# Kernel tuning notes

Measured on AMD Instinct MI355X. Metric: run time of the kernel, lower is better.

The kernel has to match this reference:

```python
import jax, jax.numpy as jnp
import numpy as np

N_HEAD = 16
N_KV_HEADS = 4
N_REP = 4
HEAD_DIM = 128
N_EMBD = 2048
EPS = 1e-5
ROPE_BASE = 10000.0


def setup_inputs() -> dict:
    key = jax.random.key(0)
    ks = jax.random.split(key, 5)
    B, T, C = 2, 2048, N_EMBD
    s = 0.02
    return {
        "x": jax.random.normal(ks[0], (B, T, C), dtype=jnp.float32),
        "wq": jax.random.normal(ks[1], (C, N_HEAD * HEAD_DIM), dtype=jnp.float32) * s,
        "wk": jax.random.normal(ks[2], (C, N_KV_HEADS * HEAD_DIM), dtype=jnp.float32) * s,
        "wv": jax.random.normal(ks[3], (C, N_KV_HEADS * HEAD_DIM), dtype=jnp.float32) * s,
        "wc": jax.random.normal(ks[4], (C, C), dtype=jnp.float32) * s,
        "q_norm_w": jnp.ones((HEAD_DIM,), dtype=jnp.float32),
        "k_norm_w": jnp.ones((HEAD_DIM,), dtype=jnp.float32),
    }


def _rmsnorm(x, w):
    # norm in fp32, scale by weight (matches RMSNorm.forward)
    xf = x.astype(jnp.float32)
    rms = jax.lax.rsqrt(jnp.mean(xf * xf, axis=-1, keepdims=True) + EPS)
    return (xf * rms).astype(x.dtype) * w


def _rope(x, cos, sin):
    # x: [B,T,H,D]; cos/sin: [T, D//2]; interleaved even/odd rotation
    xf = x.astype(jnp.float32)
    xe = xf[..., 0::2]
    xo = xf[..., 1::2]
    c = cos[None, :, None, :]
    s = sin[None, :, None, :]
    ye = xe * c - xo * s
    yo = xe * s + xo * c
    y = jnp.stack((ye, yo), axis=-1).reshape(x.shape)
    return y.astype(x.dtype)


def reference(x, wq, wk, wv, wc, q_norm_w, k_norm_w):
    B, T, C = x.shape
    q = (x @ wq).reshape(B, T, N_HEAD, HEAD_DIM)
    k = (x @ wk).reshape(B, T, N_KV_HEADS, HEAD_DIM)
    v = (x @ wv).reshape(B, T, N_KV_HEADS, HEAD_DIM)

    q = _rmsnorm(q, q_norm_w)
    k = _rmsnorm(k, k_norm_w)

    inv_freq = 1.0 / (ROPE_BASE ** (jnp.arange(0, HEAD_DIM, 2, dtype=jnp.float32) / HEAD_DIM))
    theta = jnp.arange(T, dtype=jnp.float32)[:, None] * inv_freq[None, :]  # [T, D//2]
    cos, sin = jnp.cos(theta), jnp.sin(theta)
    q = _rope(q, cos, sin)
    k = _rope(k, cos, sin)

    # GQA: repeat kv heads (repeat_kv with n_rep)
    k = jnp.repeat(k, N_REP, axis=2)  # [B,T,H,D]
    v = jnp.repeat(v, N_REP, axis=2)

    scale = 1.0 / jnp.sqrt(jnp.float32(HEAD_DIM))
    scores = jnp.einsum("bthd,bshd->bhts", q, k) * scale  # [B,H,T,S]
    causal = jnp.tril(jnp.ones((T, T), dtype=bool))
    scores = jnp.where(causal[None, None], scores, jnp.finfo(scores.dtype).min)
    attn = jax.nn.softmax(scores, axis=-1)
    y = jnp.einsum("bhts,bshd->bthd", attn, v).reshape(B, T, C)
    return y @ wc
```

## Files before the change

kernel.cpp:

```cpp
#include <hip/hip_runtime.h>
#include <hip/hip_bf16.h>
#include <cstdint>
#include <cstddef>

using bf16 = __hip_bfloat16;
typedef __attribute__((ext_vector_type(8))) short short8;
typedef __attribute__((ext_vector_type(4))) float f32x4;
typedef __attribute__((ext_vector_type(16))) float f32x16;

#define T_SEQ 2048
#define NHEAD 16
#define NKV 4
#define HD 128
#define CE 2048

__device__ __forceinline__ void gl_lds16(const void* g, void* l) {
  __builtin_amdgcn_global_load_lds(
      (const __attribute__((address_space(1))) unsigned int*)g,
      (__attribute__((address_space(3))) unsigned int*)l, 16, 0, 0);
}

__device__ __forceinline__ unsigned int cvtpk_bf16(float lo, float hi) {
  unsigned int r;
  asm("v_cvt_pk_bf16_f32 %0, %1, %2" : "=v"(r) : "v"(lo), "v"(hi));
  return r;
}

__device__ __forceinline__ void plswap(unsigned int& x, unsigned int& y, int hi) {
#if __has_builtin(__builtin_amdgcn_permlane32_swap)
  auto r = __builtin_amdgcn_permlane32_swap(x, y, false, false);
  x = r[0];
  y = r[1];
#else
  unsigned int xp = (unsigned int)__shfl_xor((int)x, 32);
  unsigned int yp = (unsigned int)__shfl_xor((int)y, 32);
  unsigned int nx = hi ? yp : x;
  unsigned int ny = hi ? y : xp;
  x = nx;
  y = ny;
#endif
}

__global__ void __launch_bounds__(256) cvt_bf16(const float* __restrict__ in,
                                                bf16* __restrict__ out, int n4) {
  const int i = blockIdx.x * blockDim.x + threadIdx.x;
  if (i >= n4) return;
  const float4 v = ((const float4*)in)[i];
  bf16 b0 = __float2bfloat16(v.x), b1 = __float2bfloat16(v.y),
       b2 = __float2bfloat16(v.z), b3 = __float2bfloat16(v.w);
  ushort4 u;
  u.x = *(const unsigned short*)&b0; u.y = *(const unsigned short*)&b1;
  u.z = *(const unsigned short*)&b2; u.w = *(const unsigned short*)&b3;
  ((ushort4*)out)[i] = u;
}

__global__ void __launch_bounds__(256) transpose_cvt(const float* __restrict__ W,
                                                     bf16* __restrict__ Wt, int N) {
  __shared__ float tile[32][33];
  const int tx = threadIdx.x & 31, ty = threadIdx.x >> 5;
  const int bx = blockIdx.x, by = blockIdx.y;
#pragma unroll
  for (int i = 0; i < 4; i++) {
    const int r = by * 32 + ty + i * 8;
    tile[ty + i * 8][tx] = W[(size_t)r * N + bx * 32 + tx];
  }
  __syncthreads();
#pragma unroll
  for (int i = 0; i < 4; i++) {
    const int n = bx * 32 + ty + i * 8;
    Wt[(size_t)n * 2048 + by * 32 + tx] = __float2bfloat16(tile[tx][ty + i * 8]);
  }
}

template <int BM, int BN, int WM, int WN, bool OBF>
__global__ void __launch_bounds__(512, 2)
gemm8i(const bf16* __restrict__ A, const bf16* __restrict__ Bt,
       void* __restrict__ Cv, int M, int N, int K) {
  constexpr int AWS = BM / 2 / WM;
  constexpr int BWS = BN / 2 / WN;
  constexpr int MH = AWS / 16;
  constexpr int NH = BWS / 16;
  constexpr int AH = BM / 128;
  constexpr int BH = BN / 128;
  constexpr int G = 2 * AH + BH;
  __shared__ bf16 smA[2][BM * 64];
  __shared__ bf16 smB[2][BN * 64];

  const int tid = threadIdx.x, lane = tid & 63, wid = tid >> 6;
  const int l15 = lane & 15, l4 = lane >> 4;
  const int wr = wid / WN, wc = wid % WN;

  const int nwg = gridDim.x;
  const int q = nwg >> 3, r = nwg & 7;
  const int xcd = blockIdx.x & 7, lin = blockIdx.x >> 3;
  const int wg = (xcd < r ? xcd * (q + 1) : r * (q + 1) + (xcd - r) * q) + lin;
  const int gw = N / BN;
  const int by = wg / gw, bx = wg % gw;
  const int row0 = by * BM, col0 = bx * BN;
  const int NT = K >> 6;
  const int NI = NT >> 1;

  const bf16* Ag = A + (size_t)row0 * K;
  const bf16* Bg = Bt + (size_t)col0 * K;

  auto stA = [&](int t, int h, int pb) {
    const int k0 = t << 6;
#pragma unroll
    for (int j = 0; j < AH; j++) {
      const int c = (h * AH + j) * 512 + tid;
      const int rowi = c >> 3;
      gl_lds16(Ag + (size_t)rowi * K + k0 + (((c & 7) ^ (rowi & 7)) << 3),
               (void*)(&smA[pb][(size_t)c << 3]));
    }
  };
  auto stB = [&](int t, int h, int pb) {
    const int k0 = t << 6;
#pragma unroll
    for (int j = 0; j < BH; j++) {
      const int c = (h * BH + j) * 512 + tid;
      const int rowi = c >> 3;
      gl_lds16(Bg + (size_t)rowi * K + k0 + (((c & 7) ^ (rowi & 7)) << 3),
               (void*)(&smB[pb][(size_t)c << 3]));
    }
  };
  auto rdA = [&](const bf16* sA, int mh, short8 (&dst)[MH][2]) {
#pragma unroll
    for (int i = 0; i < MH; i++) {
      const int rowl = mh * (BM / 2) + wr * AWS + i * 16 + l15;
#pragma unroll
      for (int kk = 0; kk < 2; kk++)
        dst[i][kk] = *(const short8*)(sA + rowl * 64 +
                                      ((((kk << 2) | l4) ^ (rowl & 7)) << 3));
    }
  };
  auto rdB = [&](const bf16* sB, int nh, short8 (&dst)[NH][2]) {
#pragma unroll
    for (int j = 0; j < NH; j++) {
      const int rowl = nh * (BN / 2) + wc * BWS + j * 16 + l15;
#pragma unroll
      for (int kk = 0; kk < 2; kk++)
        dst[j][kk] = *(const short8*)(sB + rowl * 64 +
                                      ((((kk << 2) | l4) ^ (rowl & 7)) << 3));
    }
  };

  f32x4 acc[2][2][MH][NH];
#pragma unroll
  for (int mh = 0; mh < 2; mh++)
#pragma unroll
    for (int nh = 0; nh < 2; nh++)
#pragma unroll
      for (int i = 0; i < MH; i++)
#pragma unroll
        for (int j = 0; j < NH; j++) acc[mh][nh][i][j] = (f32x4){0.f, 0.f, 0.f, 0.f};

  auto mmq = [&](short8 (&a)[MH][2], short8 (&b)[NH][2], f32x4 (&ac)[MH][NH]) {
    __builtin_amdgcn_s_setprio(1);
#pragma unroll
    for (int i = 0; i < MH; i++)
#pragma unroll
      for (int j = 0; j < NH; j++)
#pragma unroll
        for (int kk = 0; kk < 2; kk++)
          ac[i][j] = __builtin_amdgcn_mfma_f32_16x16x32_bf16(a[i][kk], b[j][kk],
                                                             ac[i][j], 0, 0, 0);
    __builtin_amdgcn_s_setprio(0);
  };

  short8 a0[MH][2], a1[MH][2], b0[NH][2], b1[NH][2];

#define LGKM0_SB                                            \
  asm volatile("s_waitcnt lgkmcnt(0)" ::: "memory");        \
  __builtin_amdgcn_sched_barrier(0);
#define GATE_G                                              \
  asm volatile("s_waitcnt vmcnt(%0)" ::"i"(G) : "memory");

  stA(0, 0, 0); stB(0, 0, 0); stA(0, 1, 0); stB(0, 1, 0);
  stA(1, 0, 1); stB(1, 0, 1); stA(1, 1, 1);
  GATE_G
  __builtin_amdgcn_s_barrier();

  for (int i = 0; i < NI - 1; ++i) {
    const int u = 2 * i, v = u + 1;
    stB(v, 1, 1);
    rdA(smA[0], 0, a0); rdB(smB[0], 0, b0);
    __builtin_amdgcn_s_barrier();
    LGKM0_SB
    mmq(a0, b0, acc[0][0]);
    __builtin_amdgcn_s_barrier();
    stA(u + 2, 0, 0);
    rdA(smA[0], 1, a1);
    __builtin_amdgcn_s_barrier();
    LGKM0_SB
    mmq(a1, b0, acc[1][0]);
    __builtin_amdgcn_s_barrier();
    stB(u + 2, 0, 0);
    rdB(smB[0], 1, b1);
    __builtin_amdgcn_s_barrier();
    LGKM0_SB
    mmq(a1, b1, acc[1][1]);
    __builtin_amdgcn_s_barrier();
    stA(u + 2, 1, 0);
    mmq(a0, b1, acc[0][1]);
    GATE_G
    __builtin_amdgcn_s_barrier();
    stB(u + 2, 1, 0);
    rdA(smA[1], 0, a0); rdB(smB[1], 0, b0);
    __builtin_amdgcn_s_barrier();
    LGKM0_SB
    mmq(a0, b0, acc[0][0]);
    __builtin_amdgcn_s_barrier();
    stA(v + 2, 0, 1);
    rdA(smA[1], 1, a1);
    __builtin_amdgcn_s_barrier();
    LGKM0_SB
    mmq(a1, b0, acc[1][0]);
    __builtin_amdgcn_s_barrier();
    stB(v + 2, 0, 1);
    rdB(smB[1], 1, b1);
    __builtin_amdgcn_s_barrier();
    LGKM0_SB
    mmq(a1, b1, acc[1][1]);
    __builtin_amdgcn_s_barrier();
    stA(v + 2, 1, 1);
    mmq(a0, b1, acc[0][1]);
    GATE_G
    __builtin_amdgcn_s_barrier();
  }

  {
    stB(NT - 1, 1, 1);
    rdA(smA[0], 0, a0); rdB(smB[0], 0, b0);
    __builtin_amdgcn_s_barrier();
    LGKM0_SB
    mmq(a0, b0, acc[0][0]);
    __builtin_amdgcn_s_barrier();
    rdA(smA[0], 1, a1);
    __builtin_amdgcn_s_barrier();
    LGKM0_SB
    mmq(a1, b0, acc[1][0]);
    __builtin_amdgcn_s_barrier();
    rdB(smB[0], 1, b1);
    __builtin_amdgcn_s_barrier();
    LGKM0_SB
    mmq(a1, b1, acc[1][1]);
    __builtin_amdgcn_s_barrier();
    mmq(a0, b1, acc[0][1]);
    asm volatile("s_waitcnt vmcnt(0)" ::: "memory");
    __builtin_amdgcn_s_barrier();
    rdA(smA[1], 0, a0); rdB(smB[1], 0, b0);
    __builtin_amdgcn_s_barrier();
    LGKM0_SB
    mmq(a0, b0, acc[0][0]);
    __builtin_amdgcn_s_barrier();
    rdA(smA[1], 1, a1);
    __builtin_amdgcn_s_barrier();
    LGKM0_SB
    mmq(a1, b0, acc[1][0]);
    __builtin_amdgcn_s_barrier();
    rdB(smB[1], 1, b1);
    __builtin_amdgcn_s_barrier();
    LGKM0_SB
    mmq(a1, b1, acc[1][1]);
    mmq(a0, b1, acc[0][1]);
  }

#pragma unroll
  for (int mh = 0; mh < 2; mh++)
#pragma unroll
    for (int nh = 0; nh < 2; nh++)
#pragma unroll
      for (int i = 0; i < MH; i++)
#pragma unroll
        for (int j = 0; j < NH; j++)
#pragma unroll
          for (int rr = 0; rr < 4; rr++) {
            const size_t row = row0 + mh * (BM / 2) + wr * AWS + i * 16 + l4 * 4 + rr;
            const size_t col = col0 + nh * (BN / 2) + wc * BWS + j * 16 + l15;
            if constexpr (OBF)
              ((bf16*)Cv)[row * N + col] = __float2bfloat16(acc[mh][nh][i][j][rr]);
            else
              ((float*)Cv)[row * N + col] = acc[mh][nh][i][j][rr];
          }
#undef LGKM0_SB
#undef GATE_G
}

__global__ void __launch_bounds__(256) qkv_post(const bf16* __restrict__ QKV,
                                                const float* __restrict__ qw,
                                                const float* __restrict__ kw,
                                                bf16* __restrict__ Qo,
                                                bf16* __restrict__ Ko,
                                                bf16* __restrict__ Vto) {
  const int g = blockIdx.x * 4 + (threadIdx.x >> 6);
  const int lane = threadIdx.x & 63;
  const int hh = g % 24;
  const int bt = g / 24;
  const int b = bt >> 11, t = bt & (T_SEQ - 1);
  int off;
  if (hh < 16) off = hh * 128;
  else if (hh < 20) off = 2048 + (hh - 16) * 128;
  else off = 2560 + (hh - 20) * 128;
  const ushort2 xr = *(const ushort2*)(QKV + (size_t)bt * 3072 + off + lane * 2);
  const float xx = __bfloat162float(*(const bf16*)&xr.x);
  const float xy = __bfloat162float(*(const bf16*)&xr.y);
  if (hh < 20) {
    float ss = xx * xx + xy * xy;
    ss += __shfl_xor(ss, 1);  ss += __shfl_xor(ss, 2);  ss += __shfl_xor(ss, 4);
    ss += __shfl_xor(ss, 8);  ss += __shfl_xor(ss, 16); ss += __shfl_xor(ss, 32);
    const float rms = rsqrtf(ss * (1.0f / 128.0f) + 1e-5f);
    const float* w = (hh < 16) ? qw : kw;
    const float x0 = xx * rms * w[lane * 2];
    const float x1 = xy * rms * w[lane * 2 + 1];
    const float inv = exp2f((float)lane * (-13.287712379549449f / 64.0f));
    const float th = (float)t * inv;
    const float sn = sinf(th), cs = cosf(th);
    const float y0 = x0 * cs - x1 * sn;
    const float y1 = x0 * sn + x1 * cs;
    const bf16 o0 = __float2bfloat16(y0), o1 = __float2bfloat16(y1);
    if (hh < 16) {
      bf16* d = Qo + ((size_t)(b * NHEAD + hh) * T_SEQ + t) * HD + lane * 2;
      d[0] = o0; d[1] = o1;
    } else {
      bf16* d = Ko + ((size_t)(b * NKV + (hh - 16)) * T_SEQ + t) * HD + lane * 2;
      d[0] = o0; d[1] = o1;
    }
  } else {
    bf16* d = Vto + ((size_t)(b * NKV + (hh - 20)) * HD + lane * 2) * T_SEQ + t;
    d[0] = __float2bfloat16(xx);
    d[T_SEQ] = __float2bfloat16(xy);
  }
}

__constant__ unsigned short JT[24] = {
    0x0807, 0x180F, 0x288F, 0x287E,
    0x0706, 0x170D, 0x277D, 0x170E, 0x276C,
    0x0605, 0x160B, 0x266B, 0x160C, 0x265A,
    0x0504, 0x1509, 0x2559, 0x150A, 0x2548,
    0x0403, 0x1408,
    0x0302, 0x0201, 0x0100};

#define ATTN_CL 0.12754125f

__global__ void __launch_bounds__(256, 2) attn_fwd(const bf16* __restrict__ Q,
                                                   const bf16* __restrict__ K,
                                                   const bf16* __restrict__ Vt,
                                                   bf16* __restrict__ Y,
                                                   float* __restrict__ PO,
                                                   float* __restrict__ PML) {
  __shared__ bf16 smK[128 * 128];
  __shared__ bf16 smV[128 * 128];

  const int bid = blockIdx.x;
  const int bh = bid & 31;
  const int jobi = bid >> 5;
  const unsigned int e = JT[jobi];
  const int jq = e & 15;
  const int lo = (e >> 4) & 15;
  const int len = (e >> 8) & 15;
  const int part = e >> 12;
  const int hi_t = lo + len;

  const int h = bh & (NHEAD - 1), b = bh >> 4;
  const int bkv = b * NKV + (h >> 2);

  const int tid = threadIdx.x, wid = tid >> 6, lane = tid & 63;
  const int l31 = lane & 31, hi = lane >> 5;
  const int q0w = jq * 128 + wid * 32;
  const int trow = tid >> 4, tslot = tid & 15;

  const bf16* Kb = K + (size_t)bkv * T_SEQ * HD;
  const bf16* Vb = Vt + (size_t)bkv * HD * T_SEQ;

  const bf16* Qrow = Q + ((size_t)bh * T_SEQ + q0w + l31) * HD + hi * 8;
  short8 qf[8];
#pragma unroll
  for (int ds = 0; ds < 8; ds++) qf[ds] = *(const short8*)(Qrow + ds * 16);

  f32x16 o[4];
#pragma unroll
  for (int d = 0; d < 4; d++) o[d] = (f32x16)(0.f);
  float mrun = -INFINITY, lrun = 0.f;

  constexpr float CL = ATTN_CL;

  for (int t = lo; t < hi_t; t++) {
    const int k0 = t * 128;
    __syncthreads();
#pragma unroll
    for (int i = 0; i < 8; i++) {
      const int row = i * 16 + trow;
      const int ss = (tslot ^ (row & 15)) * 8;
      gl_lds16(Kb + (size_t)(k0 + row) * HD + ss, (void*)((char*)smK + i * 4096 + wid * 1024));
      gl_lds16(Vb + (size_t)row * T_SEQ + k0 + ss, (void*)((char*)smV + i * 4096 + wid * 1024));
    }
    __syncthreads();

    const bool diag = (t == jq);
    const int glim = diag ? wid : 3;

    f32x16 sg[4];
#pragma unroll
    for (int g = 0; g < 4; g++) {
      if (g > glim) continue;
      f32x16 acc = (f32x16)(0.f);
#pragma unroll
      for (int ds = 0; ds < 8; ds++) {
        const int row = g * 32 + l31;
        const short8 kf = *(const short8*)(smK + (size_t)row * 128 +
                                           (((ds << 1) | hi) ^ (row & 15)) * 8);
        acc = __builtin_amdgcn_mfma_f32_32x32x16_bf16(kf, qf[ds], acc, 0, 0, 0);
      }
      sg[g] = acc;
    }
    float tmax = -INFINITY;
#pragma unroll
    for (int g = 0; g < 4; g++) {
      if (g > glim) continue;
      if (diag && g == wid) {
#pragma unroll
        for (int r = 0; r < 16; r++) {
          const int kr = (r & 3) + 8 * (r >> 2) + (hi << 2);
          if (kr > l31) sg[g][r] = -INFINITY;
        }
      }
#pragma unroll
      for (int r = 0; r < 16; r++) tmax = fmaxf(tmax, sg[g][r]);
    }
    tmax = fmaxf(tmax, __shfl_xor(tmax, 32));
    const float mnew = fmaxf(mrun, tmax);
    const float f = exp2f((mrun - mnew) * CL);
    mrun = mnew;
    lrun *= f;
#pragma unroll
    for (int d = 0; d < 4; d++)
#pragma unroll
      for (int r = 0; r < 16; r++) o[d][r] *= f;

    float lsum = 0.f;
#pragma unroll
    for (int g = 0; g < 4; g++) {
      if (g > glim) continue;
      float pp[16];
      float s0 = 0.f, s1 = 0.f;
#pragma unroll
      for (int r = 0; r < 16; r++) pp[r] = exp2f((sg[g][r] - mnew) * CL);
#pragma unroll
      for (int r = 0; r < 8; r++) { s0 += pp[2 * r]; s1 += pp[2 * r + 1]; }
      lsum += s0 + s1;

      unsigned int w0 = cvtpk_bf16(pp[0], pp[1]),  w2 = cvtpk_bf16(pp[4], pp[5]);
      unsigned int w1 = cvtpk_bf16(pp[2], pp[3]),  w3 = cvtpk_bf16(pp[6], pp[7]);
      unsigned int w4 = cvtpk_bf16(pp[8], pp[9]),  w6 = cvtpk_bf16(pp[12], pp[13]);
      unsigned int w5 = cvtpk_bf16(pp[10], pp[11]), w7 = cvtpk_bf16(pp[14], pp[15]);
      plswap(w0, w2, hi); plswap(w1, w3, hi);
      plswap(w4, w6, hi); plswap(w5, w7, hi);
      union { unsigned int u[4]; short8 s8; } pa0, pa1;
      pa0.u[0] = w0; pa0.u[1] = w1; pa0.u[2] = w2; pa0.u[3] = w3;
      pa1.u[0] = w4; pa1.u[1] = w5; pa1.u[2] = w6; pa1.u[3] = w7;

#pragma unroll
      for (int d = 0; d < 4; d++) {
        const int row = d * 32 + l31;
        const int ks0 = g * 2, ks1 = g * 2 + 1;
        const short8 vf0 = *(const short8*)(smV + (size_t)row * 128 +
                                            (((ks0 << 1) | hi) ^ (row & 15)) * 8);
        const short8 vf1 = *(const short8*)(smV + (size_t)row * 128 +
                                            (((ks1 << 1) | hi) ^ (row & 15)) * 8);
        o[d] = __builtin_amdgcn_mfma_f32_32x32x16_bf16(vf0, pa0.s8, o[d], 0, 0, 0);
        o[d] = __builtin_amdgcn_mfma_f32_32x32x16_bf16(vf1, pa1.s8, o[d], 0, 0, 0);
      }
    }
    lrun += lsum + __shfl_xor(lsum, 32);
  }

  if (part == 0) {
    const float inv = 1.0f / lrun;
    bf16* yrow = Y + ((size_t)(b * T_SEQ + q0w + l31)) * CE + h * HD;
#pragma unroll
    for (int d = 0; d < 4; d++) {
#pragma unroll
      for (int rg = 0; rg < 4; rg++) {
        ushort4 u;
        bf16 e0 = __float2bfloat16(o[d][rg * 4 + 0] * inv);
        bf16 e1 = __float2bfloat16(o[d][rg * 4 + 1] * inv);
        bf16 e2 = __float2bfloat16(o[d][rg * 4 + 2] * inv);
        bf16 e3 = __float2bfloat16(o[d][rg * 4 + 3] * inv);
        u.x = *(const unsigned short*)&e0; u.y = *(const unsigned short*)&e1;
        u.z = *(const unsigned short*)&e2; u.w = *(const unsigned short*)&e3;
        *(ushort4*)(yrow + d * 32 + rg * 8 + (hi << 2)) = u;
      }
    }
  } else {
    const int pidx = (bh * 8 + (jq - 8)) * 2 + (part - 1);
    float* po = PO + (size_t)pidx * 16384;
    const int row = wid * 32 + l31;
#pragma unroll
    for (int d = 0; d < 4; d++) {
#pragma unroll
      for (int rg = 0; rg < 4; rg++) {
        float4 v;
        v.x = o[d][rg * 4 + 0]; v.y = o[d][rg * 4 + 1];
        v.z = o[d][rg * 4 + 2]; v.w = o[d][rg * 4 + 3];
        *(float4*)(po + (size_t)row * 128 + d * 32 + rg * 8 + (hi << 2)) = v;
      }
    }
    if (hi == 0) {
      PML[(size_t)pidx * 256 + row * 2 + 0] = mrun;
      PML[(size_t)pidx * 256 + row * 2 + 1] = lrun;
    }
  }
}

__global__ void __launch_bounds__(256) attn_combine(const float* __restrict__ PO,
                                                    const float* __restrict__ PML,
                                                    bf16* __restrict__ Y) {
  const int bid = blockIdx.x;
  const int tI = bid >> 5;
  const int rg = bid & 31;
  const int tid = threadIdx.x;
  const int row = rg * 4 + (tid >> 6);
  const int c = (tid & 63) * 2;
  const int bh = tI >> 3;
  const int jq = (tI & 7) + 8;
  const int b = bh >> 4, h = bh & 15;
  const int p0 = tI * 2, p1 = p0 + 1;

  const float m0 = PML[(size_t)p0 * 256 + row * 2 + 0];
  const float l0 = PML[(size_t)p0 * 256 + row * 2 + 1];
  const float m1 = PML[(size_t)p1 * 256 + row * 2 + 0];
  const float l1 = PML[(size_t)p1 * 256 + row * 2 + 1];
  const float m = fmaxf(m0, m1);
  const float w0 = exp2f((m0 - m) * ATTN_CL);
  const float w1 = exp2f((m1 - m) * ATTN_CL);
  const float inv = 1.0f / (l0 * w0 + l1 * w1);

  const float2 a = *(const float2*)(PO + (size_t)p0 * 16384 + (size_t)row * 128 + c);
  const float2 bb = *(const float2*)(PO + (size_t)p1 * 16384 + (size_t)row * 128 + c);
  const float y0 = (a.x * w0 + bb.x * w1) * inv;
  const float y1 = (a.y * w0 + bb.y * w1) * inv;

  const int qrow = jq * 128 + row;
  bf16 e0 = __float2bfloat16(y0), e1 = __float2bfloat16(y1);
  ushort2 u;
  u.x = *(const unsigned short*)&e0;
  u.y = *(const unsigned short*)&e1;
  *(ushort2*)(Y + ((size_t)(b * T_SEQ + qrow)) * CE + h * HD + c) = u;
}

extern "C" void kernel_launch(void* const* d_in, const int* in_sizes, int n_in,
                              void* d_out, int out_size, void* d_ws, size_t ws_size,
                              hipStream_t stream) {
  const float* x   = (const float*)d_in[0];
  const float* wq  = (const float*)d_in[1];
  const float* wk  = (const float*)d_in[2];
  const float* wv  = (const float*)d_in[3];
  const float* wc  = (const float*)d_in[4];
  const float* qnw = (const float*)d_in[5];
  const float* knw = (const float*)d_in[6];
  float* out = (float*)d_out;

  char* ws = (char*)d_ws;
  bf16*  xb    = (bf16*)(ws);
  bf16*  wqkvt = (bf16*)(ws + 16777216);
  bf16*  wct   = (bf16*)(ws + 29360128);
  bf16*  qkv   = (bf16*)(ws + 37748736);
  float* partO = (float*)(ws + 37748736);
  float* partML= (float*)(ws + 71303168);
  bf16*  Qb    = (bf16*)(ws + 88080384);
  bf16*  Kb    = (bf16*)(ws + 104857600);
  bf16*  Vtb   = (bf16*)(ws + 109051904);
  bf16*  yb    = (bf16*)(ws + 113246208);

  cvt_bf16<<<8192, 256, 0, stream>>>(x, xb, 2097152);
  transpose_cvt<<<dim3(64, 64), 256, 0, stream>>>(wq, wqkvt, 2048);
  transpose_cvt<<<dim3(16, 64), 256, 0, stream>>>(wk, wqkvt + (size_t)2048 * 2048, 512);
  transpose_cvt<<<dim3(16, 64), 256, 0, stream>>>(wv, wqkvt + (size_t)2560 * 2048, 512);
  transpose_cvt<<<dim3(64, 64), 256, 0, stream>>>(wc, wct, 2048);
  gemm8i<256, 256, 2, 4, true><<<192, 512, 0, stream>>>(xb, wqkvt, qkv, 4096, 3072, 2048);
  qkv_post<<<24576, 256, 0, stream>>>(qkv, qnw, knw, Qb, Kb, Vtb);
  attn_fwd<<<768, 256, 0, stream>>>(Qb, Kb, Vtb, yb, partO, partML);
  attn_combine<<<8192, 256, 0, stream>>>(partO, partML, yb);
  gemm8i<128, 256, 2, 4, false><<<256, 512, 0, stream>>>(yb, wct, out, 4096, 2048, 2048);
}
```

Measured before the change: 230.6 us.

## Process 256 query rows per attention block with lazy softmax rescaling

Each attention block now covers 256 query rows, two 32-row sub-tiles per wave, so every K/V tile loaded into LDS feeds twice as many MFMAs. The job table, split-KV partial indexing and the combine kernel are rebuilt for the new tile size, and the grid halves to 384 blocks. Online softmax now rescales per 32-key group and skips the O rescale unless the running max grows past a threshold. MFMA sections are also wrapped in s_setprio. The cost is more accumulator registers (two O tiles per wave) and fewer blocks, which may hurt occupancy and load balance.

```diff
diff --git a/kernel.cpp b/kernel.cpp
--- a/kernel.cpp
+++ b/kernel.cpp
@@ -332,15 +332,41 @@
   }
 }
 
-__constant__ unsigned short JT[24] = {
-    0x0807, 0x180F, 0x288F, 0x287E,
-    0x0706, 0x170D, 0x277D, 0x170E, 0x276C,
-    0x0605, 0x160B, 0x266B, 0x160C, 0x265A,
-    0x0504, 0x1509, 0x2559, 0x150A, 0x2548,
-    0x0403, 0x1408,
-    0x0302, 0x0201, 0x0100};
+__constant__ unsigned short JT[12] = {
+    0x0403, 0x0C07, 0x1447,
+    0x0B86, 0x13BE,
+    0x0302, 0x0B05, 0x1335,
+    0x0A84, 0x12AC,
+    0x0201, 0x0100};
 
 #define ATTN_CL 0.12754125f
+
+#define SOFTMAX_G(ACC, MM, LL, OO, PA0, PA1)                                   \
+  {                                                                            \
+    float tmax = ACC[0];                                                       \
+    _Pragma("unroll") for (int r = 1; r < 16; r++) tmax = fmaxf(tmax, ACC[r]); \
+    tmax = fmaxf(tmax, __shfl_xor(tmax, 32));                                  \
+    if (!__all(tmax - MM <= 94.0f)) {                                          \
+      const float mnew = fmaxf(MM, tmax);                                      \
+      const float f = exp2f((MM - mnew) * ATTN_CL);                            \
+      LL *= f;                                                                 \
+      _Pragma("unroll") for (int d = 0; d < 4; d++)                            \
+      _Pragma("unroll") for (int r = 0; r < 16; r++) OO[d][r] *= f;            \
+      MM = mnew;                                                               \
+    }                                                                          \
+    float pp[16];                                                              \
+    _Pragma("unroll") for (int r = 0; r < 16; r++)                             \
+      pp[r] = exp2f((ACC[r] - MM) * ATTN_CL);                                  \
+    _Pragma("unroll") for (int r = 0; r < 16; r++) LL += pp[r];                \
+    unsigned int w0 = cvtpk_bf16(pp[0], pp[1]), w2 = cvtpk_bf16(pp[4], pp[5]); \
+    unsigned int w1 = cvtpk_bf16(pp[2], pp[3]), w3 = cvtpk_bf16(pp[6], pp[7]); \
+    unsigned int w4 = cvtpk_bf16(pp[8], pp[9]), w6 = cvtpk_bf16(pp[12], pp[13]); \
+    unsigned int w5 = cvtpk_bf16(pp[10], pp[11]), w7 = cvtpk_bf16(pp[14], pp[15]); \
+    plswap(w0, w2, hi); plswap(w1, w3, hi);                                    \
+    plswap(w4, w6, hi); plswap(w5, w7, hi);                                    \
+    PA0.u[0] = w0; PA0.u[1] = w1; PA0.u[2] = w2; PA0.u[3] = w3;                \
+    PA1.u[0] = w4; PA1.u[1] = w5; PA1.u[2] = w6; PA1.u[3] = w7;                \
+  }
 
 __global__ void __launch_bounds__(256, 2) attn_fwd(const bf16* __restrict__ Q,
                                                    const bf16* __restrict__ K,
@@ -355,10 +381,10 @@
   const int bh = bid & 31;
   const int jobi = bid >> 5;
   const unsigned int e = JT[jobi];
-  const int jq = e & 15;
-  const int lo = (e >> 4) & 15;
-  const int len = (e >> 8) & 15;
-  const int part = e >> 12;
+  const int J = e & 7;
+  const int lo = (e >> 3) & 15;
+  const int len = (e >> 7) & 15;
+  const int part = (e >> 11) & 3;
   const int hi_t = lo + len;
 
   const int h = bh & (NHEAD - 1), b = bh >> 4;
@@ -366,23 +392,28 @@
 
   const int tid = threadIdx.x, wid = tid >> 6, lane = tid & 63;
   const int l31 = lane & 31, hi = lane >> 5;
-  const int q0w = jq * 128 + wid * 32;
+  const int qb0 = J * 256 + wid * 64;
+  const int qb1 = qb0 + 32;
   const int trow = tid >> 4, tslot = tid & 15;
 
   const bf16* Kb = K + (size_t)bkv * T_SEQ * HD;
   const bf16* Vb = Vt + (size_t)bkv * HD * T_SEQ;
 
-  const bf16* Qrow = Q + ((size_t)bh * T_SEQ + q0w + l31) * HD + hi * 8;
-  short8 qf[8];
-#pragma unroll
-  for (int ds = 0; ds < 8; ds++) qf[ds] = *(const short8*)(Qrow + ds * 16);
-
-  f32x16 o[4];
-#pragma unroll
-  for (int d = 0; d < 4; d++) o[d] = (f32x16)(0.f);
-  float mrun = -INFINITY, lrun = 0.f;
-
-  constexpr float CL = ATTN_CL;
+  const bf16* Qr0 = Q + ((size_t)bh * T_SEQ + qb0 + l31) * HD + hi * 8;
+  const bf16* Qr1 = Q + ((size_t)bh * T_SEQ + qb1 + l31) * HD + hi * 8;
+  short8 qf0[8], qf1[8];
+#pragma unroll
+  for (int ds = 0; ds < 8; ds++) {
+    qf0[ds] = *(const short8*)(Qr0 + ds * 16);
+    qf1[ds] = *(const short8*)(Qr1 + ds * 16);
+  }
+
+  f32x16 o0[4], o1[4];
+#pragma unroll
+  for (int d = 0; d < 4; d++) { o0[d] = (f32x16)(0.f); o1[d] = (f32x16)(0.f); }
+  float m0 = -INFINITY, l0 = 0.f, m1 = -INFINITY, l1 = 0.f;
+
+  union PAu { unsigned int u[4]; short8 s8; };
 
   for (int t = lo; t < hi_t; t++) {
     const int k0 = t * 128;
@@ -396,118 +427,126 @@
     }
     __syncthreads();
 
-    const bool diag = (t == jq);
-    const int glim = diag ? wid : 3;
-
-    f32x16 sg[4];
 #pragma unroll
     for (int g = 0; g < 4; g++) {
-      if (g > glim) continue;
-      f32x16 acc = (f32x16)(0.f);
-#pragma unroll
-      for (int ds = 0; ds < 8; ds++) {
-        const int row = g * 32 + l31;
-        const short8 kf = *(const short8*)(smK + (size_t)row * 128 +
-                                           (((ds << 1) | hi) ^ (row & 15)) * 8);
-        acc = __builtin_amdgcn_mfma_f32_32x32x16_bf16(kf, qf[ds], acc, 0, 0, 0);
+      const int kb = k0 + g * 32;
+      const bool a1 = (kb <= qb1);
+      const bool a0 = (kb <= qb0);
+      if (!a1) continue;
+
+      f32x16 acc0 = (f32x16)(0.f), acc1 = (f32x16)(0.f);
+      const int row = g * 32 + l31;
+      __builtin_amdgcn_s_setprio(1);
+      if (a0) {
+#pragma unroll
+        for (int ds = 0; ds < 8; ds++) {
+          const short8 kf = *(const short8*)(smK + (size_t)row * 128 +
+                                             ((((ds << 1) | hi) ^ (row & 15)) << 3));
+          acc0 = __builtin_amdgcn_mfma_f32_32x32x16_bf16(kf, qf0[ds], acc0, 0, 0, 0);
+          acc1 = __builtin_amdgcn_mfma_f32_32x32x16_bf16(kf, qf1[ds], acc1, 0, 0, 0);
+        }
+      } else {
+#pragma unroll
+        for (int ds = 0; ds < 8; ds++) {
+          const short8 kf = *(const short8*)(smK + (size_t)row * 128 +
+                                             ((((ds << 1) | hi) ^ (row & 15)) << 3));
+          acc1 = __builtin_amdgcn_mfma_f32_32x32x16_bf16(kf, qf1[ds], acc1, 0, 0, 0);
+        }
       }
-      sg[g] = acc;
-    }
-    float tmax = -INFINITY;
-#pragma unroll
-    for (int g = 0; g < 4; g++) {
-      if (g > glim) continue;
-      if (diag && g == wid) {
+      __builtin_amdgcn_s_setprio(0);
+
+      if (kb == qb0) {
 #pragma unroll
         for (int r = 0; r < 16; r++) {
           const int kr = (r & 3) + 8 * (r >> 2) + (hi << 2);
-          if (kr > l31) sg[g][r] = -INFINITY;
+          if (kr > l31) acc0[r] = -INFINITY;
         }
       }
-#pragma unroll
-      for (int r = 0; r < 16; r++) tmax = fmaxf(tmax, sg[g][r]);
-    }
-    tmax = fmaxf(tmax, __shfl_xor(tmax, 32));
-    const float mnew = fmaxf(mrun, tmax);
-    const float f = exp2f((mrun - mnew) * CL);
-    mrun = mnew;
-    lrun *= f;
-#pragma unroll
-    for (int d = 0; d < 4; d++)
-#pragma unroll
-      for (int r = 0; r < 16; r++) o[d][r] *= f;
-
-    float lsum = 0.f;
-#pragma unroll
-    for (int g = 0; g < 4; g++) {
-      if (g > glim) continue;
-      float pp[16];
-      float s0 = 0.f, s1 = 0.f;
-#pragma unroll
-      for (int r = 0; r < 16; r++) pp[r] = exp2f((sg[g][r] - mnew) * CL);
-#pragma unroll
-      for (int r = 0; r < 8; r++) { s0 += pp[2 * r]; s1 += pp[2 * r + 1]; }
-      lsum += s0 + s1;
-
-      unsigned int w0 = cvtpk_bf16(pp[0], pp[1]),  w2 = cvtpk_bf16(pp[4], pp[5]);
-      unsigned int w1 = cvtpk_bf16(pp[2], pp[3]),  w3 = cvtpk_bf16(pp[6], pp[7]);
-      unsigned int w4 = cvtpk_bf16(pp[8], pp[9]),  w6 = cvtpk_bf16(pp[12], pp[13]);
-      unsigned int w5 = cvtpk_bf16(pp[10], pp[11]), w7 = cvtpk_bf16(pp[14], pp[15]);
-      plswap(w0, w2, hi); plswap(w1, w3, hi);
-      plswap(w4, w6, hi); plswap(w5, w7, hi);
-      union { unsigned int u[4]; short8 s8; } pa0, pa1;
-      pa0.u[0] = w0; pa0.u[1] = w1; pa0.u[2] = w2; pa0.u[3] = w3;
-      pa1.u[0] = w4; pa1.u[1] = w5; pa1.u[2] = w6; pa1.u[3] = w7;
-
+      if (kb == qb1) {
+#pragma unroll
+        for (int r = 0; r < 16; r++) {
+          const int kr = (r & 3) + 8 * (r >> 2) + (hi << 2);
+          if (kr > l31) acc1[r] = -INFINITY;
+        }
+      }
+
+      PAu pa00, pa01, pa10, pa11;
+      if (a0) SOFTMAX_G(acc0, m0, l0, o0, pa00, pa01);
+      SOFTMAX_G(acc1, m1, l1, o1, pa10, pa11);
+
+      __builtin_amdgcn_s_setprio(1);
 #pragma unroll
       for (int d = 0; d < 4; d++) {
-        const int row = d * 32 + l31;
-        const int ks0 = g * 2, ks1 = g * 2 + 1;
-        const short8 vf0 = *(const short8*)(smV + (size_t)row * 128 +
-                                            (((ks0 << 1) | hi) ^ (row & 15)) * 8);
-        const short8 vf1 = *(const short8*)(smV + (size_t)row * 128 +
-                                            (((ks1 << 1) | hi) ^ (row & 15)) * 8);
-        o[d] = __builtin_amdgcn_mfma_f32_32x32x16_bf16(vf0, pa0.s8, o[d], 0, 0, 0);
-        o[d] = __builtin_amdgcn_mfma_f32_32x32x16_bf16(vf1, pa1.s8, o[d], 0, 0, 0);
+        const int vrow = d * 32 + l31;
+        const int ks0 = g * 2, ks1 = ks0 + 1;
+        const short8 vf0 = *(const short8*)(smV + (size_t)vrow * 128 +
+                                            ((((ks0 << 1) | hi) ^ (vrow & 15)) << 3));
+        const short8 vf1 = *(const short8*)(smV + (size_t)vrow * 128 +
+                                            ((((ks1 << 1) | hi) ^ (vrow & 15)) << 3));
+        if (a0) {
+          o0[d] = __builtin_amdgcn_mfma_f32_32x32x16_bf16(vf0, pa00.s8, o0[d], 0, 0, 0);
+          o0[d] = __builtin_amdgcn_mfma_f32_32x32x16_bf16(vf1, pa01.s8, o0[d], 0, 0, 0);
+        }
+        o1[d] = __builtin_amdgcn_mfma_f32_32x32x16_bf16(vf0, pa10.s8, o1[d], 0, 0, 0);
+        o1[d] = __builtin_amdgcn_mfma_f32_32x32x16_bf16(vf1, pa11.s8, o1[d], 0, 0, 0);
       }
-    }
-    lrun += lsum + __shfl_xor(lsum, 32);
-  }
+      __builtin_amdgcn_s_setprio(0);
+    }
+  }
+
+  const float lt0 = l0 + __shfl_xor(l0, 32);
+  const float lt1 = l1 + __shfl_xor(l1, 32);
 
   if (part == 0) {
-    const float inv = 1.0f / lrun;
-    bf16* yrow = Y + ((size_t)(b * T_SEQ + q0w + l31)) * CE + h * HD;
+    const float inv0 = 1.0f / lt0;
+    const float inv1 = 1.0f / lt1;
+    bf16* yr0 = Y + ((size_t)(b * T_SEQ + qb0 + l31)) * CE + h * HD;
+    bf16* yr1 = Y + ((size_t)(b * T_SEQ + qb1 + l31)) * CE + h * HD;
 #pragma unroll
     for (int d = 0; d < 4; d++) {
 #pragma unroll
       for (int rg = 0; rg < 4; rg++) {
-        ushort4 u;
-        bf16 e0 = __float2bfloat16(o[d][rg * 4 + 0] * inv);
-        bf16 e1 = __float2bfloat16(o[d][rg * 4 + 1] * inv);
-        bf16 e2 = __float2bfloat16(o[d][rg * 4 + 2] * inv);
-        bf16 e3 = __float2bfloat16(o[d][rg * 4 + 3] * inv);
-        u.x = *(const unsigned short*)&e0; u.y = *(const unsigned short*)&e1;
-        u.z = *(const unsigned short*)&e2; u.w = *(const unsigned short*)&e3;
-        *(ushort4*)(yrow + d * 32 + rg * 8 + (hi << 2)) = u;
+        ushort4 u0, u1;
+        bf16 e0, e1, e2, e3;
+        e0 = __float2bfloat16(o0[d][rg * 4 + 0] * inv0);
+        e1 = __float2bfloat16(o0[d][rg * 4 + 1] * inv0);
+        e2 = __float2bfloat16(o0[d][rg * 4 + 2] * inv0);
+        e3 = __float2bfloat16(o0[d][rg * 4 + 3] * inv0);
+        u0.x = *(const unsigned short*)&e0; u0.y = *(const unsigned short*)&e1;
+        u0.z = *(const unsigned short*)&e2; u0.w = *(const unsigned short*)&e3;
+        *(ushort4*)(yr0 + d * 32 + rg * 8 + (hi << 2)) = u0;
+        e0 = __float2bfloat16(o1[d][rg * 4 + 0] * inv1);
+        e1 = __float2bfloat16(o1[d][rg * 4 + 1] * inv1);
+        e2 = __float2bfloat16(o1[d][rg * 4 + 2] * inv1);
+        e3 = __float2bfloat16(o1[d][rg * 4 + 3] * inv1);
+        u1.x = *(const unsigned short*)&e0; u1.y = *(const unsigned short*)&e1;
+        u1.z = *(const unsigned short*)&e2; u1.w = *(const unsigned short*)&e3;
+        *(ushort4*)(yr1 + d * 32 + rg * 8 + (hi << 2)) = u1;
       }
     }
   } else {
-    const int pidx = (bh * 8 + (jq - 8)) * 2 + (part - 1);
-    float* po = PO + (size_t)pidx * 16384;
-    const int row = wid * 32 + l31;
+    const int pidx = (bh * 4 + (J - 4)) * 2 + (part - 1);
+    float* po = PO + (size_t)pidx * 32768;
+    const int r0 = wid * 64 + l31;
+    const int r1 = r0 + 32;
 #pragma unroll
     for (int d = 0; d < 4; d++) {
 #pragma unroll
       for (int rg = 0; rg < 4; rg++) {
-        float4 v;
-        v.x = o[d][rg * 4 + 0]; v.y = o[d][rg * 4 + 1];
-        v.z = o[d][rg * 4 + 2]; v.w = o[d][rg * 4 + 3];
-        *(float4*)(po + (size_t)row * 128 + d * 32 + rg * 8 + (hi << 2)) = v;
+        float4 v0, v1;
+        v0.x = o0[d][rg * 4 + 0]; v0.y = o0[d][rg * 4 + 1];
+        v0.z = o0[d][rg * 4 + 2]; v0.w = o0[d][rg * 4 + 3];
+        *(float4*)(po + (size_t)r0 * 128 + d * 32 + rg * 8 + (hi << 2)) = v0;
+        v1.x = o1[d][rg * 4 + 0]; v1.y = o1[d][rg * 4 + 1];
+        v1.z = o1[d][rg * 4 + 2]; v1.w = o1[d][rg * 4 + 3];
+        *(float4*)(po + (size_t)r1 * 128 + d * 32 + rg * 8 + (hi << 2)) = v1;
       }
     }
     if (hi == 0) {
-      PML[(size_t)pidx * 256 + row * 2 + 0] = mrun;
-      PML[(size_t)pidx * 256 + row * 2 + 1] = lrun;
+      PML[(size_t)pidx * 512 + r0 * 2 + 0] = m0;
+      PML[(size_t)pidx * 512 + r0 * 2 + 1] = lt0;
+      PML[(size_t)pidx * 512 + r1 * 2 + 0] = m1;
+      PML[(size_t)pidx * 512 + r1 * 2 + 1] = lt1;
     }
   }
 }
@@ -516,31 +555,31 @@
                                                     const float* __restrict__ PML,
                                                     bf16* __restrict__ Y) {
   const int bid = blockIdx.x;
-  const int tI = bid >> 5;
-  const int rg = bid & 31;
+  const int tI = bid >> 6;
+  const int rg = bid & 63;
   const int tid = threadIdx.x;
   const int row = rg * 4 + (tid >> 6);
   const int c = (tid & 63) * 2;
-  const int bh = tI >> 3;
-  const int jq = (tI & 7) + 8;
+  const int bh = tI >> 2;
+  const int J = (tI & 3) + 4;
   const int b = bh >> 4, h = bh & 15;
   const int p0 = tI * 2, p1 = p0 + 1;
 
-  const float m0 = PML[(size_t)p0 * 256 + row * 2 + 0];
-  const float l0 = PML[(size_t)p0 * 256 + row * 2 + 1];
-  const float m1 = PML[(size_t)p1 * 256 + row * 2 + 0];
-  const float l1 = PML[(size_t)p1 * 256 + row * 2 + 1];
+  const float m0 = PML[(size_t)p0 * 512 + row * 2 + 0];
+  const float l0 = PML[(size_t)p0 * 512 + row * 2 + 1];
+  const float m1 = PML[(size_t)p1 * 512 + row * 2 + 0];
+  const float l1 = PML[(size_t)p1 * 512 + row * 2 + 1];
   const float m = fmaxf(m0, m1);
   const float w0 = exp2f((m0 - m) * ATTN_CL);
   const float w1 = exp2f((m1 - m) * ATTN_CL);
   const float inv = 1.0f / (l0 * w0 + l1 * w1);
 
-  const float2 a = *(const float2*)(PO + (size_t)p0 * 16384 + (size_t)row * 128 + c);
-  const float2 bb = *(const float2*)(PO + (size_t)p1 * 16384 + (size_t)row * 128 + c);
+  const float2 a = *(const float2*)(PO + (size_t)p0 * 32768 + (size_t)row * 128 + c);
+  const float2 bb = *(const float2*)(PO + (size_t)p1 * 32768 + (size_t)row * 128 + c);
   const float y0 = (a.x * w0 + bb.x * w1) * inv;
   const float y1 = (a.y * w0 + bb.y * w1) * inv;
 
-  const int qrow = jq * 128 + row;
+  const int qrow = J * 256 + row;
   bf16 e0 = __float2bfloat16(y0), e1 = __float2bfloat16(y1);
   ushort2 u;
   u.x = *(const unsigned short*)&e0;
@@ -579,7 +618,7 @@
   transpose_cvt<<<dim3(64, 64), 256, 0, stream>>>(wc, wct, 2048);
   gemm8i<256, 256, 2, 4, true><<<192, 512, 0, stream>>>(xb, wqkvt, qkv, 4096, 3072, 2048);
   qkv_post<<<24576, 256, 0, stream>>>(qkv, qnw, knw, Qb, Kb, Vtb);
-  attn_fwd<<<768, 256, 0, stream>>>(Qb, Kb, Vtb, yb, partO, partML);
+  attn_fwd<<<384, 256, 0, stream>>>(Qb, Kb, Vtb, yb, partO, partML);
   attn_combine<<<8192, 256, 0, stream>>>(partO, partML, yb);
   gemm8i<128, 256, 2, 4, false><<<256, 512, 0, stream>>>(yb, wct, out, 4096, 2048, 2048);
 }
```

New measurement: 286.2 us. 1.24x slower.
